# Optimization experiments

Measured on AMD Instinct MI355X. Metric: run time of the kernel, lower is better.

## Reference

```python
import jax, jax.numpy as jnp
import numpy as np

N_USER = 50000
N_ITEM = 30000
NNZ = 500000  # user-item interactions; edges duplicated symmetrically -> E = 2*NNZ
EMB = 64
N_LAYERS = 2
N_FACTORS = 4
N_ITERATIONS = 2


def setup_inputs() -> dict:
    key = jax.random.key(0)
    k1, k2, k3, k4 = jax.random.split(key, 4)
    user_emb = jax.random.normal(k1, (N_USER, EMB), dtype=jnp.float32) * 0.1
    item_emb = jax.random.normal(k2, (N_ITEM, EMB), dtype=jnp.float32) * 0.1
    row = jax.random.randint(k3, (NNZ,), 0, N_USER, dtype=jnp.int32)
    col = jax.random.randint(k4, (NNZ,), 0, N_ITEM, dtype=jnp.int32) + N_USER
    # symmetric edge list exactly as the torch module builds it
    all_h_list = jnp.concatenate([row, col], axis=0)
    all_t_list = jnp.concatenate([col, row], axis=0)
    return {"user_emb": user_emb, "item_emb": item_emb,
            "all_h_list": all_h_list, "all_t_list": all_t_list}


def _dgcf_forward(user_emb, item_emb, all_h_list, all_t_list):
    n_user = user_emb.shape[0]
    ego = jnp.concatenate([user_emb, item_emb], axis=0)  # [N, D]
    N, D = ego.shape
    F = N_FACTORS
    d = D // F
    E = all_h_list.shape[0]
    dtype = ego.dtype

    all_embeddings = [ego]
    A = jnp.ones((E, F), dtype=dtype)  # A_values init

    for _layer in range(N_LAYERS):
        # torch.chunk along dim 1 == reshape [N, F, d]
        chunks = ego.reshape(N, F, d)
        tail_chunks = chunks[all_t_list]  # [E, F, d] gather of tail embeddings
        factor_emb = None
        for _t in range(N_ITERATIONS):
            # build_matrix, vectorized over the F factors
            normA = jax.nn.softmax(A, axis=1)                        # [E, F]
            dval = jax.ops.segment_sum(normA, all_h_list, num_segments=N)  # [N, F]
            dinv = 1.0 / jnp.sqrt(jnp.clip(dval, 1e-8))
            edge_weight = normA * dinv[all_h_list] * dinv[all_t_list]  # [E, F]
            # message passing per factor: gather tail, weight, scatter to head
            edge_val = tail_chunks * edge_weight[:, :, None]           # [E, F, d]
            factor_emb = jax.ops.segment_sum(edge_val, all_h_list, num_segments=N)  # [N, F, d]
            # dynamic routing update of A
            head = factor_emb[all_h_list]                              # [E, F, d]
            head = head / jnp.clip(jnp.linalg.norm(head, axis=-1, keepdims=True), 1e-12)
            tail = tail_chunks / jnp.clip(jnp.linalg.norm(tail_chunks, axis=-1, keepdims=True), 1e-12)
            A_iter = jnp.sum(head * jnp.tanh(tail), axis=-1)           # [E, F]
            A = A + A_iter
        ego = factor_emb.reshape(N, D)  # concat of factor chunks (last iteration)
        all_embeddings.append(ego)

    all_emb = jnp.mean(jnp.stack(all_embeddings, axis=1), axis=1)  # [N, D]
    return all_emb[:n_user], all_emb[n_user:]


def reference(user_emb, item_emb, all_h_list, all_t_list):
    return _dgcf_forward(user_emb, item_emb, all_h_list, all_t_list)
```

## Files before the change

kernel.cpp:

```cpp
#include <hip/hip_runtime.h>
#include <hip/hip_bf16.h>

#define N_USER 50000
#define N_ITEM 30000
#define NTOT   80000
#define EMB    64
#define FAC    4
#define EDGES  1000000
#define LOG4   1.3862943611198906f
#define NBUCK  512
#define BBLK   512
#define BCH    1954


__device__ inline float bf2f(unsigned short u) {
    return __uint_as_float(((unsigned int)u) << 16);
}
__device__ inline unsigned short f2bf(float f) {
    unsigned int x = __float_as_uint(f);
    x += 0x7FFFu + ((x >> 16) & 1u);
    return (unsigned short)(x >> 16);
}
__device__ inline float dot2(unsigned int a, unsigned int b) {
    float a0 = __uint_as_float(a << 16), a1 = __uint_as_float(a & 0xFFFF0000u);
    float b0 = __uint_as_float(b << 16), b1 = __uint_as_float(b & 0xFFFF0000u);
    return a0 * b0 + a1 * b1;
}
__device__ inline int bucket_of(int h) { return (int)(((unsigned)h * NBUCK) / (unsigned)NTOT); }
__device__ inline int bucket_lo(int k) { return (k * NTOT + NBUCK - 1) / NBUCK; }

__global__ void k_detect(const unsigned short* __restrict__ raw, int* __restrict__ flag) {
    __shared__ int s;
    if (threadIdx.x == 0) s = 0;
    __syncthreads();
    int c = 0;
    for (int i = threadIdx.x; i < 16384; i += 256) {
        unsigned short u = raw[i];
        if ((u & 0x7F80) == 0x7F80) c++;
    }
    atomicAdd(&s, c);
    __syncthreads();
    if (threadIdx.x == 0) *flag = (s > 0) ? 1 : 0;
}

__global__ void k_init(const void* __restrict__ ue, const void* __restrict__ ie,
                       const int* __restrict__ flag,
                       unsigned short* __restrict__ egoh,
                       unsigned short* __restrict__ tnh0) {
    int gid = blockIdx.x * blockDim.x + threadIdx.x;
    int wid = gid >> 6;
    int lane = threadIdx.x & 63;
    if (wid >= NTOT) return;
    int i = wid * 64 + lane;
    bool isf32 = (*flag != 0);
    float v;
    if (i < N_USER * EMB) {
        v = isf32 ? ((const float*)ue)[i]
                  : __bfloat162float(((const __hip_bfloat16*)ue)[i]);
    } else {
        int j = i - N_USER * EMB;
        v = isf32 ? ((const float*)ie)[j]
                  : __bfloat162float(((const __hip_bfloat16*)ie)[j]);
    }
    egoh[i] = f2bf(v);
    float ss = v * v;
    ss += __shfl_xor(ss, 1); ss += __shfl_xor(ss, 2);
    ss += __shfl_xor(ss, 4); ss += __shfl_xor(ss, 8);
    float rr = 1.0f / fmaxf(sqrtf(ss), 1e-12f);
    tnh0[i] = f2bf(tanhf(v * rr));
}

__global__ void k_bcnt(const int* __restrict__ hl, int* __restrict__ cnt) {
    __shared__ int hist[NBUCK];
    int b = blockIdx.x, tid = threadIdx.x;
    for (int i = tid; i < NBUCK; i += 256) hist[i] = 0;
    __syncthreads();
    int base = b * BCH, end = base + BCH; if (end > EDGES) end = EDGES;
    for (int e = base + tid; e < end; e += 256)
        atomicAdd(&hist[bucket_of(hl[e])], 1);
    __syncthreads();
    for (int i = tid; i < NBUCK; i += 256) cnt[b * NBUCK + i] = hist[i];
}

__global__ void k_btot(const int* __restrict__ cnt, int* __restrict__ boff) {
    __shared__ int sbuf[NBUCK];
    int k = threadIdx.x;
    int s = 0;
    for (int b = 0; b < BBLK; ++b) s += cnt[b * NBUCK + k];
    sbuf[k] = s;
    __syncthreads();
    int v = s;
    for (int st = 1; st < NBUCK; st <<= 1) {
        int t = (k >= st) ? sbuf[k - st] : 0;
        __syncthreads();
        sbuf[k] += t;
        __syncthreads();
    }
    boff[k] = sbuf[k] - v;
    if (k == NBUCK - 1) boff[NBUCK] = EDGES;
}

__global__ void k_bscan(const int* __restrict__ cnt, const int* __restrict__ boff,
                        int* __restrict__ gbase) {
    __shared__ int buf[BBLK];
    int k = blockIdx.x, tid = threadIdx.x;
    int v = cnt[tid * NBUCK + k];
    buf[tid] = v;
    __syncthreads();
    for (int s = 1; s < BBLK; s <<= 1) {
        int t = (tid >= s) ? buf[tid - s] : 0;
        __syncthreads();
        buf[tid] += t;
        __syncthreads();
    }
    gbase[tid * NBUCK + k] = boff[k] + buf[tid] - v;
}

__global__ void k_bscat(const int* __restrict__ hl, const int* __restrict__ tl,
                        const int* __restrict__ gbase, int* __restrict__ bt) {
    __shared__ int lg[NBUCK];
    int b = blockIdx.x, tid = threadIdx.x;
    for (int i = tid; i < NBUCK; i += 256) lg[i] = gbase[b * NBUCK + i];
    __syncthreads();
    int base = b * BCH, end = base + BCH; if (end > EDGES) end = EDGES;
    for (int e = base + tid; e < end; e += 256) {
        int h = hl[e];
        int k = bucket_of(h);
        int pos = atomicAdd(&lg[k], 1);
        bt[pos] = ((h - bucket_lo(k)) << 17) | tl[e];
    }
}

__global__ void k_bfin(const int* __restrict__ bt, const int* __restrict__ boff,
                       int* __restrict__ off, float* __restrict__ dvacc,
                       int* __restrict__ tlist, int* __restrict__ hlist) {
    __shared__ int ldeg[160];
    __shared__ int lcur[160];
    __shared__ int sbuf[256];
    int k = blockIdx.x, tid = threadIdx.x;
    int lo = bucket_lo(k), hi = bucket_lo(k + 1);
    int nn = hi - lo;
    for (int i = tid; i < nn; i += 256) ldeg[i] = 0;
    __syncthreads();
    int start = boff[k], end = boff[k + 1];
    for (int j = start + tid; j < end; j += 256)
        atomicAdd(&ldeg[bt[j] >> 17], 1);
    __syncthreads();
    int v = (tid < nn) ? ldeg[tid] : 0;
    sbuf[tid] = v;
    __syncthreads();
    for (int s = 1; s < 256; s <<= 1) {
        int t = (tid >= s) ? sbuf[tid - s] : 0;
        __syncthreads();
        sbuf[tid] += t;
        __syncthreads();
    }
    if (tid < nn) {
        int o = start + sbuf[tid] - v;
        off[lo + tid] = o;
        lcur[tid] = o;
        float d = 0.25f * (float)v;
        ((float4*)dvacc)[lo + tid] = make_float4(d, d, d, d);
    }
    if (k == 0 && tid == 0) off[NTOT] = EDGES;
    __syncthreads();
    for (int j = start + tid; j < end; j += 256) {
        int val = bt[j];
        int hrel = val >> 17;
        int t = val & 0x1FFFF;
        int pos = atomicAdd(&lcur[hrel], 1);
        tlist[pos] = t;
        hlist[pos] = lo + hrel;
    }
}

__global__ void k_scale(float* __restrict__ dvacc, float* __restrict__ dvinv,
                        const unsigned short* __restrict__ ego,
                        unsigned short* __restrict__ egoS) {
    int gid = blockIdx.x * blockDim.x + threadIdx.x;
    int wid = gid >> 6;
    int lane = threadIdx.x & 63;
    if (wid >= NTOT) return;
    int f = lane >> 4;
    float r = rsqrtf(fmaxf(dvacc[wid * 4 + f], 1e-8f));
    if ((lane & 15) == 0) dvinv[wid * 4 + f] = r;
    if (lane < 4) dvacc[wid * 4 + lane] = 0.f;
    int i = wid * 64 + lane;
    egoS[i] = f2bf(bf2f(ego[i]) * r);
}

__global__ void k_mp(const unsigned short* __restrict__ egoS, const float* __restrict__ P,
                     const float* __restrict__ dvinv, const int* __restrict__ off,
                     const int* __restrict__ tlist,
                     unsigned short* __restrict__ fach, float* __restrict__ rhn,
                     unsigned short* __restrict__ tnhOut,
                     const unsigned short* __restrict__ f1b,
                     const void* __restrict__ ue, const void* __restrict__ ie,
                     const int* __restrict__ flag, float* __restrict__ outF,
                     int useP, int writeRhn, int writeTnh, int doFinal) {
    int gid = blockIdx.x * blockDim.x + threadIdx.x;
    int wid = gid >> 6;
    int lane = threadIdx.x & 63;
    if (wid >= NTOT) return;
    int c = lane & 15;
    int q = lane >> 4;
    int f = c >> 2;
    int beg = off[wid], end = off[wid + 1];
    float dvh = dvinv[wid * 4 + f];
    const uint2* eg2 = (const uint2*)egoS;

    float a0 = 0.f, a1 = 0.f, a2 = 0.f, a3 = 0.f;
    int nfull = (end - beg) >> 2;
    int j = beg + q;
    if (useP) {
#pragma unroll 2
        for (int g = 0; g < nfull; ++g, j += 4) {
            int t = tlist[j];
            float w = P[j * 4 + f];
            uint2 u = eg2[t * 16 + c];
            a0 += w * __uint_as_float(u.x << 16);
            a1 += w * __uint_as_float(u.x & 0xFFFF0000u);
            a2 += w * __uint_as_float(u.y << 16);
            a3 += w * __uint_as_float(u.y & 0xFFFF0000u);
        }
        if (j < end) {
            int t = tlist[j];
            float w = P[j * 4 + f];
            uint2 u = eg2[t * 16 + c];
            a0 += w * __uint_as_float(u.x << 16);
            a1 += w * __uint_as_float(u.x & 0xFFFF0000u);
            a2 += w * __uint_as_float(u.y << 16);
            a3 += w * __uint_as_float(u.y & 0xFFFF0000u);
        }
    } else {
#pragma unroll 2
        for (int g = 0; g < nfull; ++g, j += 4) {
            int t = tlist[j];
            uint2 u = eg2[t * 16 + c];
            a0 += __uint_as_float(u.x << 16);
            a1 += __uint_as_float(u.x & 0xFFFF0000u);
            a2 += __uint_as_float(u.y << 16);
            a3 += __uint_as_float(u.y & 0xFFFF0000u);
        }
        if (j < end) {
            int t = tlist[j];
            uint2 u = eg2[t * 16 + c];
            a0 += __uint_as_float(u.x << 16);
            a1 += __uint_as_float(u.x & 0xFFFF0000u);
            a2 += __uint_as_float(u.y << 16);
            a3 += __uint_as_float(u.y & 0xFFFF0000u);
        }
        a0 *= 0.25f; a1 *= 0.25f; a2 *= 0.25f; a3 *= 0.25f;
    }

    a0 += __shfl_xor(a0, 16); a1 += __shfl_xor(a1, 16);
    a2 += __shfl_xor(a2, 16); a3 += __shfl_xor(a3, 16);
    a0 += __shfl_xor(a0, 32); a1 += __shfl_xor(a1, 32);
    a2 += __shfl_xor(a2, 32); a3 += __shfl_xor(a3, 32);

    a0 *= dvh; a1 *= dvh; a2 *= dvh; a3 *= dvh;

    if (doFinal) {
        if (q == 0) {
            bool isf32 = (*flag != 0);
            float i0, i1, i2, i3;
            if (wid < N_USER) {
                if (isf32) {
                    float4 t4 = ((const float4*)ue)[wid * 16 + c];
                    i0 = t4.x; i1 = t4.y; i2 = t4.z; i3 = t4.w;
                } else {
                    uint2 t2 = ((const uint2*)ue)[wid * 16 + c];
                    i0 = __uint_as_float(t2.x << 16); i1 = __uint_as_float(t2.x & 0xFFFF0000u);
                    i2 = __uint_as_float(t2.y << 16); i3 = __uint_as_float(t2.y & 0xFFFF0000u);
                }
            } else {
                int w2 = wid - N_USER;
                if (isf32) {
                    float4 t4 = ((const float4*)ie)[w2 * 16 + c];
                    i0 = t4.x; i1 = t4.y; i2 = t4.z; i3 = t4.w;
                } else {
                    uint2 t2 = ((const uint2*)ie)[w2 * 16 + c];
                    i0 = __uint_as_float(t2.x << 16); i1 = __uint_as_float(t2.x & 0xFFFF0000u);
                    i2 = __uint_as_float(t2.y << 16); i3 = __uint_as_float(t2.y & 0xFFFF0000u);
                }
            }
            uint2 fr = ((const uint2*)f1b)[wid * 16 + c];
            float g0 = __uint_as_float(fr.x << 16), g1 = __uint_as_float(fr.x & 0xFFFF0000u),
                  g2 = __uint_as_float(fr.y << 16), g3 = __uint_as_float(fr.y & 0xFFFF0000u);
            const float k3 = 1.0f / 3.0f;
            ((float4*)outF)[wid * 16 + c] =
                make_float4((i0 + g0 + a0) * k3, (i1 + g1 + a1) * k3,
                            (i2 + g2 + a2) * k3, (i3 + g3 + a3) * k3);
        }
        return;
    }

    if (q == 0) {
        unsigned int p01 = (unsigned int)f2bf(a0) | ((unsigned int)f2bf(a1) << 16);
        unsigned int p23 = (unsigned int)f2bf(a2) | ((unsigned int)f2bf(a3) << 16);
        ((uint2*)fach)[wid * 16 + c] = make_uint2(p01, p23);
    }

    if (writeRhn || writeTnh) {
        float ss = a0 * a0 + a1 * a1 + a2 * a2 + a3 * a3;
        ss += __shfl_xor(ss, 1); ss += __shfl_xor(ss, 2);
        float rr = 1.0f / fmaxf(sqrtf(ss), 1e-12f);
        if (writeRhn && q == 0 && (c & 3) == 0) rhn[wid * 4 + f] = rr;
        if (writeTnh) {
            float t0 = tanhf(a0 * rr), t1 = tanhf(a1 * rr),
                  t2 = tanhf(a2 * rr), t3 = tanhf(a3 * rr);
            if (q == 0) {
                unsigned int p01 = (unsigned int)f2bf(t0) | ((unsigned int)f2bf(t1) << 16);
                unsigned int p23 = (unsigned int)f2bf(t2) | ((unsigned int)f2bf(t3) << 16);
                ((uint2*)tnhOut)[wid * 16 + c] = make_uint2(p01, p23);
            }
        }
    }
}

__global__ void k_upd(const unsigned short* __restrict__ fach,
                      const unsigned short* __restrict__ tnhh,
                      const float* __restrict__ rhn,
                      const int* __restrict__ hlist, const int* __restrict__ tlist,
                      float* __restrict__ P, float* __restrict__ dval, int first) {
    __shared__ int   s_h[256];
    __shared__ float s_p[256][4];
    int tid = threadIdx.x;
    int j = blockIdx.x * 256 + tid;
    int h = -1;
    if (j < EDGES) {
        h = hlist[j];
        int t = tlist[j];
        const uint4* frow = (const uint4*)(fach + (size_t)h * 64);
        const uint4* trow = (const uint4*)(tnhh + (size_t)t * 64);
        float d[4];
#pragma unroll
        for (int f = 0; f < 4; ++f) {
            uint4 a0 = frow[f * 2], a1 = frow[f * 2 + 1];
            uint4 b0 = trow[f * 2], b1 = trow[f * 2 + 1];
            d[f] = dot2(a0.x, b0.x) + dot2(a0.y, b0.y)
                 + dot2(a0.z, b0.z) + dot2(a0.w, b0.w)
                 + dot2(a1.x, b1.x) + dot2(a1.y, b1.y)
                 + dot2(a1.z, b1.z) + dot2(a1.w, b1.w);
        }
        float4 rh = ((const float4*)rhn)[h];
        float lx, ly, lz, lw;
        if (first) { lx = ly = lz = lw = -LOG4; }
        else {
            float4 p0 = ((const float4*)P)[j];
            lx = __logf(p0.x); ly = __logf(p0.y);
            lz = __logf(p0.z); lw = __logf(p0.w);
        }
        float y0 = lx + rh.x * d[0], y1 = ly + rh.y * d[1],
              y2 = lz + rh.z * d[2], y3 = lw + rh.w * d[3];
        float m = fmaxf(fmaxf(y0, y1), fmaxf(y2, y3));
        float e0 = __expf(y0 - m), e1 = __expf(y1 - m),
              e2 = __expf(y2 - m), e3 = __expf(y3 - m);
        float inv = 1.0f / (e0 + e1 + e2 + e3);
        float p0n = e0 * inv, p1n = e1 * inv, p2n = e2 * inv, p3n = e3 * inv;
        ((float4*)P)[j] = make_float4(p0n, p1n, p2n, p3n);
        s_p[tid][0] = p0n; s_p[tid][1] = p1n; s_p[tid][2] = p2n; s_p[tid][3] = p3n;
    }
    s_h[tid] = h;
    __syncthreads();
    if (h == -1) return;
    if (tid > 0 && s_h[tid - 1] == h) return;
    float a0 = 0.f, a1 = 0.f, a2 = 0.f, a3 = 0.f;
    int k = tid;
    while (k < 256 && s_h[k] == h) {
        a0 += s_p[k][0]; a1 += s_p[k][1]; a2 += s_p[k][2]; a3 += s_p[k][3];
        ++k;
    }
    float* dst = dval + (size_t)h * 4;
    if (tid == 0 || k == 256) {
        unsafeAtomicAdd(dst + 0, a0);
        unsafeAtomicAdd(dst + 1, a1);
        unsafeAtomicAdd(dst + 2, a2);
        unsafeAtomicAdd(dst + 3, a3);
    } else {
        ((float4*)dst)[0] = make_float4(a0, a1, a2, a3);
    }
}

extern "C" void kernel_launch(void* const* d_in, const int* in_sizes, int n_in,
                              void* d_out, int out_size, void* d_ws, size_t ws_size,
                              hipStream_t stream) {
    const void* ue = d_in[0];
    const void* ie = d_in[1];
    const int* hl = (const int*)d_in[2];
    const int* tl = (const int*)d_in[3];
    float* out = (float*)d_out;

    float* ws    = (float*)d_ws;
    float* P     = ws;
    int*   bt    = (int*)(ws);
    int*   cnt   = (int*)(ws + 1000000);
    int*   gbase = (int*)(ws + 1262144);
    float* dvacc = ws + 4000000;
    float* dvinv = ws + 4320000;
    float* rhn   = ws + 4640000;
    unsigned short* bufW = (unsigned short*)(ws + 4960000);
    unsigned short* bufX = (unsigned short*)(ws + 7520000);
    unsigned short* bufY = (unsigned short*)(ws + 10080000);
    unsigned short* bufZ0 = (unsigned short*)(ws + 12640000);
    unsigned short* bufZ1 = (unsigned short*)(ws + 15200000);
    unsigned short* egoS = (unsigned short*)(ws + 17760000);
    int*   flag = (int*)(ws + 20320000);
    int*   boff = (int*)(ws + 20320016);
    int*   off  = (int*)(ws + 20400016);
    int*   tlist = (int*)(ws + 20480017);
    int*   hlist = (int*)(ws + 21480017);

    k_detect<<<1, 256, 0, stream>>>((const unsigned short*)ue, flag);
    k_init<<<20000, 256, 0, stream>>>(ue, ie, flag, bufW, bufZ0);

    k_bcnt<<<BBLK, 256, 0, stream>>>(hl, cnt);
    k_btot<<<1, NBUCK, 0, stream>>>(cnt, boff);
    k_bscan<<<NBUCK, BBLK, 0, stream>>>(cnt, boff, gbase);
    k_bscat<<<BBLK, 256, 0, stream>>>(hl, tl, gbase, bt);
    k_bfin<<<NBUCK, 256, 0, stream>>>(bt, boff, off, dvacc, tlist, hlist);

    k_scale<<<20000, 256, 0, stream>>>(dvacc, dvinv, bufW, egoS);
    k_mp<<<20000, 256, 0, stream>>>(egoS, P, dvinv, off, tlist, bufX, rhn, bufZ1,
                                    bufY, ue, ie, flag, out,
                                    0, 1, 0, 0);
    k_upd<<<3907, 256, 0, stream>>>(bufX, bufZ0, rhn, hlist, tlist, P, dvacc, 1);
    k_scale<<<20000, 256, 0, stream>>>(dvacc, dvinv, bufW, egoS);
    k_mp<<<20000, 256, 0, stream>>>(egoS, P, dvinv, off, tlist, bufY, rhn, bufZ1,
                                    bufY, ue, ie, flag, out,
                                    1, 1, 1, 0);
    k_upd<<<3907, 256, 0, stream>>>(bufY, bufZ0, rhn, hlist, tlist, P, dvacc, 0);
    k_scale<<<20000, 256, 0, stream>>>(dvacc, dvinv, bufY, egoS);
    k_mp<<<20000, 256, 0, stream>>>(egoS, P, dvinv, off, tlist, bufX, rhn, bufZ1,
                                    bufY, ue, ie, flag, out,
                                    1, 1, 0, 0);
    k_upd<<<3907, 256, 0, stream>>>(bufX, bufZ1, rhn, hlist, tlist, P, dvacc, 0);
    k_scale<<<20000, 256, 0, stream>>>(dvacc, dvinv, bufY, egoS);
    k_mp<<<20000, 256, 0, stream>>>(egoS, P, dvinv, off, tlist, bufX, rhn, bufZ1,
                                    bufY, ue, ie, flag, out,
                                    1, 0, 0, 1);
}
```

Measured before the change: 438.0 us.

## Fuse degree scaling into message passing and ping-pong degree accumulators

```diff
diff --git a/kernel.cpp b/kernel.cpp
--- a/kernel.cpp
+++ b/kernel.cpp
@@ -174,24 +174,9 @@
     }
 }
 
-__global__ void k_scale(float* __restrict__ dvacc, float* __restrict__ dvinv,
-                        const unsigned short* __restrict__ ego,
-                        unsigned short* __restrict__ egoS) {
-    int gid = blockIdx.x * blockDim.x + threadIdx.x;
-    int wid = gid >> 6;
-    int lane = threadIdx.x & 63;
-    if (wid >= NTOT) return;
-    int f = lane >> 4;
-    float r = rsqrtf(fmaxf(dvacc[wid * 4 + f], 1e-8f));
-    if ((lane & 15) == 0) dvinv[wid * 4 + f] = r;
-    if (lane < 4) dvacc[wid * 4 + lane] = 0.f;
-    int i = wid * 64 + lane;
-    egoS[i] = f2bf(bf2f(ego[i]) * r);
-}
-
-__global__ void k_mp(const unsigned short* __restrict__ egoS, const float* __restrict__ P,
-                     const float* __restrict__ dvinv, const int* __restrict__ off,
-                     const int* __restrict__ tlist,
+__global__ void k_mp(const unsigned short* __restrict__ ego, const float* __restrict__ P,
+                     const float* __restrict__ dva, float* __restrict__ zb,
+                     const int* __restrict__ off, const int* __restrict__ tlist,
                      unsigned short* __restrict__ fach, float* __restrict__ rhn,
                      unsigned short* __restrict__ tnhOut,
                      const unsigned short* __restrict__ f1b,
@@ -205,9 +190,10 @@
     int c = lane & 15;
     int q = lane >> 4;
     int f = c >> 2;
+    if (zb != nullptr && lane < 4) zb[wid * 4 + lane] = 0.f;
     int beg = off[wid], end = off[wid + 1];
-    float dvh = dvinv[wid * 4 + f];
-    const uint2* eg2 = (const uint2*)egoS;
+    float dvh = rsqrtf(fmaxf(dva[wid * 4 + f], 1e-8f));
+    const uint2* eg2 = (const uint2*)ego;
 
     float a0 = 0.f, a1 = 0.f, a2 = 0.f, a3 = 0.f;
     int nfull = (end - beg) >> 2;
@@ -217,7 +203,9 @@
         for (int g = 0; g < nfull; ++g, j += 4) {
             int t = tlist[j];
             float w = P[j * 4 + f];
-            uint2 u = eg2[t * 16 + c];
+            float dvt = rsqrtf(fmaxf(dva[t * 4 + f], 1e-8f));
+            uint2 u = eg2[(size_t)t * 16 + c];
+            w *= dvt;
             a0 += w * __uint_as_float(u.x << 16);
             a1 += w * __uint_as_float(u.x & 0xFFFF0000u);
             a2 += w * __uint_as_float(u.y << 16);
@@ -226,7 +214,9 @@
         if (j < end) {
             int t = tlist[j];
             float w = P[j * 4 + f];
-            uint2 u = eg2[t * 16 + c];
+            float dvt = rsqrtf(fmaxf(dva[t * 4 + f], 1e-8f));
+            uint2 u = eg2[(size_t)t * 16 + c];
+            w *= dvt;
             a0 += w * __uint_as_float(u.x << 16);
             a1 += w * __uint_as_float(u.x & 0xFFFF0000u);
             a2 += w * __uint_as_float(u.y << 16);
@@ -236,21 +226,24 @@
 #pragma unroll 2
         for (int g = 0; g < nfull; ++g, j += 4) {
             int t = tlist[j];
-            uint2 u = eg2[t * 16 + c];
-            a0 += __uint_as_float(u.x << 16);
-            a1 += __uint_as_float(u.x & 0xFFFF0000u);
-            a2 += __uint_as_float(u.y << 16);
-            a3 += __uint_as_float(u.y & 0xFFFF0000u);
+            float dvt = rsqrtf(fmaxf(dva[t * 4 + f], 1e-8f));
+            uint2 u = eg2[(size_t)t * 16 + c];
+            float w = 0.25f * dvt;
+            a0 += w * __uint_as_float(u.x << 16);
+            a1 += w * __uint_as_float(u.x & 0xFFFF0000u);
+            a2 += w * __uint_as_float(u.y << 16);
+            a3 += w * __uint_as_float(u.y & 0xFFFF0000u);
         }
         if (j < end) {
             int t = tlist[j];
-            uint2 u = eg2[t * 16 + c];
-            a0 += __uint_as_float(u.x << 16);
-            a1 += __uint_as_float(u.x & 0xFFFF0000u);
-            a2 += __uint_as_float(u.y << 16);
-            a3 += __uint_as_float(u.y & 0xFFFF0000u);
-        }
-        a0 *= 0.25f; a1 *= 0.25f; a2 *= 0.25f; a3 *= 0.25f;
+            float dvt = rsqrtf(fmaxf(dva[t * 4 + f], 1e-8f));
+            uint2 u = eg2[(size_t)t * 16 + c];
+            float w = 0.25f * dvt;
+            a0 += w * __uint_as_float(u.x << 16);
+            a1 += w * __uint_as_float(u.x & 0xFFFF0000u);
+            a2 += w * __uint_as_float(u.y << 16);
+            a3 += w * __uint_as_float(u.y & 0xFFFF0000u);
+        }
     }
 
     a0 += __shfl_xor(a0, 16); a1 += __shfl_xor(a1, 16);
@@ -396,15 +389,14 @@
     int*   bt    = (int*)(ws);
     int*   cnt   = (int*)(ws + 1000000);
     int*   gbase = (int*)(ws + 1262144);
-    float* dvacc = ws + 4000000;
-    float* dvinv = ws + 4320000;
+    float* dvA   = ws + 4000000;
+    float* dvB   = ws + 4320000;
     float* rhn   = ws + 4640000;
     unsigned short* bufW = (unsigned short*)(ws + 4960000);
     unsigned short* bufX = (unsigned short*)(ws + 7520000);
     unsigned short* bufY = (unsigned short*)(ws + 10080000);
     unsigned short* bufZ0 = (unsigned short*)(ws + 12640000);
     unsigned short* bufZ1 = (unsigned short*)(ws + 15200000);
-    unsigned short* egoS = (unsigned short*)(ws + 17760000);
     int*   flag = (int*)(ws + 20320000);
     int*   boff = (int*)(ws + 20320016);
     int*   off  = (int*)(ws + 20400016);
@@ -418,25 +410,21 @@
     k_btot<<<1, NBUCK, 0, stream>>>(cnt, boff);
     k_bscan<<<NBUCK, BBLK, 0, stream>>>(cnt, boff, gbase);
     k_bscat<<<BBLK, 256, 0, stream>>>(hl, tl, gbase, bt);
-    k_bfin<<<NBUCK, 256, 0, stream>>>(bt, boff, off, dvacc, tlist, hlist);
-
-    k_scale<<<20000, 256, 0, stream>>>(dvacc, dvinv, bufW, egoS);
-    k_mp<<<20000, 256, 0, stream>>>(egoS, P, dvinv, off, tlist, bufX, rhn, bufZ1,
+    k_bfin<<<NBUCK, 256, 0, stream>>>(bt, boff, off, dvA, tlist, hlist);
+
+    k_mp<<<20000, 256, 0, stream>>>(bufW, P, dvA, dvB, off, tlist, bufX, rhn, bufZ1,
                                     bufY, ue, ie, flag, out,
                                     0, 1, 0, 0);
-    k_upd<<<3907, 256, 0, stream>>>(bufX, bufZ0, rhn, hlist, tlist, P, dvacc, 1);
-    k_scale<<<20000, 256, 0, stream>>>(dvacc, dvinv, bufW, egoS);
-    k_mp<<<20000, 256, 0, stream>>>(egoS, P, dvinv, off, tlist, bufY, rhn, bufZ1,
+    k_upd<<<3907, 256, 0, stream>>>(bufX, bufZ0, rhn, hlist, tlist, P, dvB, 1);
+    k_mp<<<20000, 256, 0, stream>>>(bufW, P, dvB, dvA, off, tlist, bufY, rhn, bufZ1,
                                     bufY, ue, ie, flag, out,
                                     1, 1, 1, 0);
-    k_upd<<<3907, 256, 0, stream>>>(bufY, bufZ0, rhn, hlist, tlist, P, dvacc, 0);
-    k_scale<<<20000, 256, 0, stream>>>(dvacc, dvinv, bufY, egoS);
-    k_mp<<<20000, 256, 0, stream>>>(egoS, P, dvinv, off, tlist, bufX, rhn, bufZ1,
+    k_upd<<<3907, 256, 0, stream>>>(bufY, bufZ0, rhn, hlist, tlist, P, dvA, 0);
+    k_mp<<<20000, 256, 0, stream>>>(bufY, P, dvA, dvB, off, tlist, bufX, rhn, bufZ1,
                                     bufY, ue, ie, flag, out,
                                     1, 1, 0, 0);
-    k_upd<<<3907, 256, 0, stream>>>(bufX, bufZ1, rhn, hlist, tlist, P, dvacc, 0);
-    k_scale<<<20000, 256, 0, stream>>>(dvacc, dvinv, bufY, egoS);
-    k_mp<<<20000, 256, 0, stream>>>(egoS, P, dvinv, off, tlist, bufX, rhn, bufZ1,
+    k_upd<<<3907, 256, 0, stream>>>(bufX, bufZ1, rhn, hlist, tlist, P, dvB, 0);
+    k_mp<<<20000, 256, 0, stream>>>(bufY, P, dvB, nullptr, off, tlist, bufX, rhn, bufZ1,
                                     bufY, ue, ie, flag, out,
                                     1, 0, 0, 1);
 }
```

After: 403.1 us. -8.0%, faster.
